# Kernel tuning notes

Measured on AMD Instinct MI355X. Metric: run time of the kernel, lower is better.

## Reference

```python
import jax, jax.numpy as jnp
import numpy as np

# Dimensions (match init_kwargs / input_specs)
B, S, D = 4, 2048, 1024
H, DK = 16, 64
CL = 64            # chunk_len
C, N, NL = 32, 2, 128  # chunks, neighbors, neighbor_len
EPS = 1e-5
SCALE = 1.0 / np.sqrt(DK)


def setup_inputs() -> dict:
    key = jax.random.key(0)
    ks = jax.random.split(key, 8)
    w_in = 1.0 / np.sqrt(D)   # xavier-like scale for projections
    return {
        "h": jax.random.normal(ks[0], (B, S, D), jnp.float32),
        "e": jax.random.normal(ks[1], (B, C, N, NL, D), jnp.float32),
        "ln_g": jnp.ones((D,), jnp.float32),
        "ln_b": jnp.zeros((D,), jnp.float32),
        "Wq": jax.random.normal(ks[2], (D, H * DK), jnp.float32) * w_in,
        "bq": jnp.zeros((H * DK,), jnp.float32),
        "Wk": jax.random.normal(ks[3], (D, H * DK), jnp.float32) * w_in,
        "bk": jnp.zeros((H * DK,), jnp.float32),
        "Wv": jax.random.normal(ks[4], (D, H * DK), jnp.float32) * w_in,
        "bv": jnp.zeros((H * DK,), jnp.float32),
        "Wo": jax.random.normal(ks[5], (H * DK, D), jnp.float32) * (1.0 / np.sqrt(H * DK)),
        "bo": jnp.zeros((D,), jnp.float32),
    }


def _layernorm(x, g, b):
    mu = jnp.mean(x, axis=-1, keepdims=True)
    var = jnp.mean(jnp.square(x - mu), axis=-1, keepdims=True)
    return (x - mu) * jax.lax.rsqrt(var + EPS) * g + b


def reference(h, e, ln_g, ln_b, Wq, bq, Wk, bk, Wv, bv, Wo, bo):
    residual = h
    # shift queries so each chunk attends to neighbors retrieved for the previous chunk
    hs = _layernorm(h[:, CL - 1:], ln_g, ln_b)          # [B, S-CL+1, D]
    total = C * CL
    pad = max(0, total - hs.shape[1])
    hp = jnp.pad(hs, ((0, 0), (0, pad), (0, 0))) if pad > 0 else hs[:, :total]
    hb = hp.reshape(B, C, CL, D)                         # [B,C,CL,D]

    q = (hb @ Wq + bq).reshape(B, C, CL, H, DK)
    k = (e @ Wk + bk).reshape(B, C, N, NL, H, DK)
    v = (e @ Wv + bv).reshape(B, C, N, NL, H, DK)

    # scores: [B, C, H, CL, N, NL], softmax over merged (N, NL)
    attn = jnp.einsum('bcihd,bcnjhd->bchinj', q, k) * SCALE
    sh = attn.shape
    attn = jax.nn.softmax(attn.reshape(sh[0], sh[1], sh[2], sh[3], -1), axis=-1).reshape(sh)

    o = jnp.einsum('bchinj,bcnjhd->bcihd', attn, v).reshape(B, C * CL, H * DK)
    o = o @ Wo + bo                                      # [B, C*CL, D]
    # shift output back and crop to original length
    o = jnp.pad(o, ((0, 0), (CL - 1, 0), (0, 0)))[:, :S]
    return o + residual
```

## Files before the change

kernel.cpp:

```cpp
#include <hip/hip_runtime.h>


typedef __attribute__((ext_vector_type(8))) short short8;
typedef __attribute__((ext_vector_type(4))) float f32x4;
typedef unsigned short ushort_t;
typedef unsigned long long u64;

__device__ inline ushort_t f2bf(float f) {
  union { float f; unsigned int u; } v; v.f = f;
  unsigned int u = v.u;
  return (ushort_t)((u + 0x7fffu + ((u >> 16) & 1u)) >> 16);
}
__device__ inline float bf2f(ushort_t s) {
  union { unsigned int u; float f; } v; v.u = ((unsigned int)s) << 16;
  return v.f;
}

__device__ inline void gl_lds16(const void* g, void* l) {
  __builtin_amdgcn_global_load_lds(
      (const __attribute__((address_space(1))) unsigned int*)g,
      (__attribute__((address_space(3))) unsigned int*)l, 16, 0, 0);
}

__global__ void prep_kernel(const float* __restrict__ W0, const float* __restrict__ W1,
                            const float* __restrict__ W2, const float* __restrict__ W3,
                            ushort_t* __restrict__ T0, ushort_t* __restrict__ T1,
                            ushort_t* __restrict__ T2, ushort_t* __restrict__ T3,
                            const float* __restrict__ h, const float* __restrict__ lg,
                            const float* __restrict__ lb, ushort_t* __restrict__ hb,
                            const float* __restrict__ e, ushort_t* __restrict__ e_bf) {
  __shared__ float tile[32][33];
  __shared__ float red[8];
  const int blk = blockIdx.x, t = threadIdx.x;

  if (blk < 4096) {
    const int z = blk >> 10, xy = blk & 1023;
    const float* W = (z == 0) ? W0 : (z == 1) ? W1 : (z == 2) ? W2 : W3;
    ushort_t* WT   = (z == 0) ? T0 : (z == 1) ? T1 : (z == 2) ? T2 : T3;
    int k0 = (xy & 31) * 32, n0 = (xy >> 5) * 32;
    int c = t & 31, r = t >> 5;
#pragma unroll
    for (int p = 0; p < 4; p++)
      tile[r + p * 8][c] = W[(size_t)(k0 + r + p * 8) * 1024 + n0 + c];
    __syncthreads();
#pragma unroll
    for (int p = 0; p < 4; p++)
      WT[(size_t)(n0 + r + p * 8) * 1024 + k0 + c] = f2bf(tile[c][r + p * 8]);
    return;
  }
  if (blk < 12288) {
    int row = blk - 4096;
    int b = row >> 11, jj = row & 2047;
    ushort_t* dst = hb + (size_t)row * 1024;
    if (jj >= 1985) {
      ((unsigned int*)dst)[t] = 0u;
      ((unsigned int*)dst)[t + 256] = 0u;
      return;
    }
    const float* src = h + ((size_t)(b << 11) + jj + 63) * 1024;
    f32x4 x = *(const f32x4*)&src[t * 4];
    float s = x[0] + x[1] + x[2] + x[3];
    float sq = x[0]*x[0] + x[1]*x[1] + x[2]*x[2] + x[3]*x[3];
#pragma unroll
    for (int off = 32; off > 0; off >>= 1) {
      s  += __shfl_xor(s, off);
      sq += __shfl_xor(sq, off);
    }
    if ((t & 63) == 0) { red[(t >> 6) * 2] = s; red[(t >> 6) * 2 + 1] = sq; }
    __syncthreads();
    float sum = red[0] + red[2] + red[4] + red[6];
    float sumsq = red[1] + red[3] + red[5] + red[7];
    float mu = sum * (1.f / 1024.f);
    float var = sumsq * (1.f / 1024.f) - mu * mu;
    float rs = rsqrtf(var + 1e-5f);
    f32x4 gg = *(const f32x4*)&lg[t * 4];
    f32x4 bv = *(const f32x4*)&lb[t * 4];
    ushort_t o0 = f2bf((x[0] - mu) * rs * gg[0] + bv[0]);
    ushort_t o1 = f2bf((x[1] - mu) * rs * gg[1] + bv[1]);
    ushort_t o2 = f2bf((x[2] - mu) * rs * gg[2] + bv[2]);
    ushort_t o3 = f2bf((x[3] - mu) * rs * gg[3] + bv[3]);
    u64 pack = (u64)o0 | ((u64)o1 << 16) | ((u64)o2 << 32) | ((u64)o3 << 48);
    *(u64*)&dst[t * 4] = pack;
    return;
  }
  {
    int i = (blk - 12288) * 256 + t;
    const f32x4* sp = (const f32x4*)(e + (size_t)i * 8);
    f32x4 a = sp[0], b = sp[1];
    short8 o;
    o[0] = (short)f2bf(a[0]); o[1] = (short)f2bf(a[1]);
    o[2] = (short)f2bf(a[2]); o[3] = (short)f2bf(a[3]);
    o[4] = (short)f2bf(b[0]); o[5] = (short)f2bf(b[1]);
    o[6] = (short)f2bf(b[2]); o[7] = (short)f2bf(b[3]);
    *(short8*)(e_bf + (size_t)i * 8) = o;
  }
}

template <int EPI>
__launch_bounds__(256, 2)
__global__ void gemm_bt(const ushort_t* __restrict__ A, const ushort_t* __restrict__ BT,
                        const float* __restrict__ bias, ushort_t* __restrict__ Cb,
                        float* __restrict__ Cf, const float* __restrict__ resid) {
  const int bid = blockIdx.x;
  if (EPI == 1 && bid >= 512) {
    int tt = bid - 512;
    int b = tt / 63, r = tt % 63;
    size_t idx = ((size_t)(b * 2048) + r) * 1024 + threadIdx.x * 4;
    *(f32x4*)&Cf[idx] = *(const f32x4*)&resid[idx];
    return;
  }
  __shared__ __attribute__((aligned(16))) ushort_t lds[32768];
  const int cpx = 64;
  const int swz = (bid & 7) * cpx + (bid >> 3);
  const int tm = (swz >> 3) * 128, tn = (swz & 7) * 128;
  const int t = threadIdx.x, lane = t & 63, wv = t >> 6;
  const int wm = (wv >> 1) * 64, wn = (wv & 1) * 64;
  const int row16 = lane & 15, g = lane >> 4;

  const int c0 = t, c1 = t + 256;
  const int ra0 = c0 >> 2, sa0 = ((c0 & 3) ^ ((ra0 >> 1) & 3)) * 8;
  const int ra1 = c1 >> 2, sa1 = ((c1 & 3) ^ ((ra1 >> 1) & 3)) * 8;
  const ushort_t* Ag0 = A + (size_t)(tm + ra0) * 1024 + sa0;
  const ushort_t* Ag1 = A + (size_t)(tm + ra1) * 1024 + sa1;
  const ushort_t* Bg0 = BT + (size_t)(tn + ra0) * 1024 + sa0;
  const ushort_t* Bg1 = BT + (size_t)(tn + ra1) * 1024 + sa1;

#define STG_A(T) { ushort_t* L_ = lds + ((T) & 3) * 8192; const int k0_ = (T) * 32; \
    gl_lds16(Ag0 + k0_, L_ + c0 * 8); gl_lds16(Ag1 + k0_, L_ + c1 * 8); }
#define STG_B(T) { ushort_t* L_ = lds + ((T) & 3) * 8192; const int k0_ = (T) * 32; \
    gl_lds16(Bg0 + k0_, L_ + 4096 + c0 * 8); gl_lds16(Bg1 + k0_, L_ + 4096 + c1 * 8); }

  int aoff[4], boff[4];
#pragma unroll
  for (int m = 0; m < 4; m++) {
    int ra = wm + m * 16 + row16;
    aoff[m] = ra * 32 + (g ^ ((ra >> 1) & 3)) * 8;
  }
#pragma unroll
  for (int n = 0; n < 4; n++) {
    int rb = wn + n * 16 + row16;
    boff[n] = 4096 + rb * 32 + (g ^ ((rb >> 1) & 3)) * 8;
  }

  f32x4 acc[4][4] = {};
  STG_A(0); STG_B(0); STG_A(1); STG_B(1);
  for (int T = 0; T < 32; ++T) {
    const ushort_t* Lb = lds + (T & 3) * 8192;
    if (T < 31) { asm volatile("s_waitcnt vmcnt(4)" ::: "memory"); }
    else        { asm volatile("s_waitcnt vmcnt(0)" ::: "memory"); }
    __builtin_amdgcn_s_barrier();
    short8 af0, af1;
    short8 bfv[4];
#pragma unroll
    for (int n = 0; n < 4; n++) bfv[n] = *(const short8*)&Lb[boff[n]];
    af0 = *(const short8*)&Lb[aoff[0]];
    af1 = *(const short8*)&Lb[aoff[1]];
    if (T < 30) STG_A(T + 2);
    __builtin_amdgcn_s_barrier();
    asm volatile("s_waitcnt lgkmcnt(0)" ::: "memory");
    __builtin_amdgcn_sched_barrier(0);
    __builtin_amdgcn_s_setprio(1);
#pragma unroll
    for (int n = 0; n < 4; n++) {
      acc[0][n] = __builtin_amdgcn_mfma_f32_16x16x32_bf16(af0, bfv[n], acc[0][n], 0, 0, 0);
      acc[1][n] = __builtin_amdgcn_mfma_f32_16x16x32_bf16(af1, bfv[n], acc[1][n], 0, 0, 0);
    }
    __builtin_amdgcn_s_setprio(0);
    __builtin_amdgcn_s_barrier();
    af0 = *(const short8*)&Lb[aoff[2]];
    af1 = *(const short8*)&Lb[aoff[3]];
    if (T < 30) STG_B(T + 2);
    __builtin_amdgcn_s_barrier();
    asm volatile("s_waitcnt lgkmcnt(0)" ::: "memory");
    __builtin_amdgcn_sched_barrier(0);
    __builtin_amdgcn_s_setprio(1);
#pragma unroll
    for (int n = 0; n < 4; n++) {
      acc[2][n] = __builtin_amdgcn_mfma_f32_16x16x32_bf16(af0, bfv[n], acc[2][n], 0, 0, 0);
      acc[3][n] = __builtin_amdgcn_mfma_f32_16x16x32_bf16(af1, bfv[n], acc[3][n], 0, 0, 0);
    }
    __builtin_amdgcn_s_setprio(0);
  }
#undef STG_A
#undef STG_B

  const int cr = g * 4, cc = row16;
  if (EPI == 0) {
    const int cb = tn + wn;
    float bsv[4];
#pragma unroll
    for (int n = 0; n < 4; n++) bsv[n] = bias[cb + n * 16 + cc];
#pragma unroll
    for (int m = 0; m < 4; m++) {
      int rbase = tm + wm + m * 16 + cr;
#pragma unroll
      for (int j = 0; j < 4; j++) {
        u64 pack = (u64)f2bf(acc[m][0][j] + bsv[0])
                 | ((u64)f2bf(acc[m][1][j] + bsv[1]) << 16)
                 | ((u64)f2bf(acc[m][2][j] + bsv[2]) << 32)
                 | ((u64)f2bf(acc[m][3][j] + bsv[3]) << 48);
        *(u64*)&Cb[(size_t)(rbase + j) * 1024 + cb + cc * 4] = pack;
      }
    }
  } else {
#pragma unroll
    for (int m = 0; m < 4; m++) {
#pragma unroll
      for (int n = 0; n < 4; n++) {
        int col = tn + wn + n * 16 + cc;
        float bsv = bias[col];
#pragma unroll
        for (int j = 0; j < 4; j++) {
          int rg = tm + wm + m * 16 + cr + j;
          float v = acc[m][n][j] + bsv;
          int b = rg >> 11, jj = rg & 2047;
          if (jj < 1985) {
            size_t oi = ((size_t)(b << 11) + jj + 63) * 1024 + col;
            Cf[oi] = v + resid[oi];
          }
        }
      }
    }
  }
}

__launch_bounds__(512, 2)
__global__ void kv_attn(const ushort_t* __restrict__ A, const ushort_t* __restrict__ WkvT,
                        const float* __restrict__ bk, const float* __restrict__ bv,
                        const ushort_t* __restrict__ Qb, ushort_t* __restrict__ Ob) {
  __shared__ __attribute__((aligned(16))) ushort_t smem[75776];
  ushort_t* lds = smem;
  const int bid = blockIdx.x;
  const int swz = (bid & 7) * 128 + (bid >> 3);
  const int bc = swz >> 3, hp = swz & 7;
  const int tm = bc * 256;
  const int t = threadIdx.x, lane = t & 63, wv = t >> 6;
  const int wm = wv >> 2, wn = wv & 3;
  const int row16 = lane & 15, g = lane >> 4;

  {
    const int hb2q = t >> 8, tlq = t & 255;
    ushort_t* QsH = smem + 67584 + hb2q * 4096;
    size_t qbase = ((size_t)bc * 64) * 1024 + (hp * 2 + hb2q) * 64;
    int ch = tlq, r = ch >> 3, gq = (ch & 7) ^ (r & 7);
    gl_lds16(Qb + qbase + (size_t)r * 1024 + gq * 8, &QsH[ch * 8]);
    ch = tlq + 256; r = ch >> 3; gq = (ch & 7) ^ (r & 7);
    gl_lds16(Qb + qbase + (size_t)r * 1024 + gq * 8, &QsH[ch * 8]);
  }

  const int d1 = t + 512;
  const int ra0 = t >> 2, sa0 = ((t & 3) ^ ((ra0 >> 1) & 3)) * 8;
  const int ra1 = d1 >> 2, sa1 = ((d1 & 3) ^ ((ra1 >> 1) & 3)) * 8;
  const ushort_t* Ag0 = A + (size_t)(tm + ra0) * 1024 + sa0;
  const ushort_t* Ag1 = A + (size_t)(tm + ra1) * 1024 + sa1;
  const ushort_t* Bg0 = WkvT + (size_t)(hp * 128 + ra0) * 1024 + sa0;
  const ushort_t* Bg1 = WkvT + (size_t)(1024 + hp * 128 + (ra1 - 128)) * 1024 + sa1;

#define STG256_A(T) { ushort_t* L_ = lds + ((T) & 3) * 16384; const int k0_ = (T) * 32; \
    gl_lds16(Ag0 + k0_, L_ + t * 8); gl_lds16(Ag1 + k0_, L_ + d1 * 8); }
#define STG256_B(T) { ushort_t* L_ = lds + ((T) & 3) * 16384; const int k0_ = (T) * 32; \
    gl_lds16(Bg0 + k0_, L_ + 8192 + t * 8); gl_lds16(Bg1 + k0_, L_ + 8192 + d1 * 8); }

  int aoff[8], boff[4];
#pragma unroll
  for (int m = 0; m < 8; m++) {
    int ra = wm * 128 + m * 16 + row16;
    aoff[m] = ra * 32 + (g ^ ((ra >> 1) & 3)) * 8;
  }
#pragma unroll
  for (int n = 0; n < 4; n++) {
    int rb = wn * 64 + n * 16 + row16;
    boff[n] = 8192 + rb * 32 + (g ^ ((rb >> 1) & 3)) * 8;
  }

  f32x4 acc[8][4] = {};
  STG256_A(0); STG256_B(0); STG256_A(1); STG256_B(1);
  for (int T = 0; T < 32; ++T) {
    const ushort_t* Lb = lds + (T & 3) * 16384;
    if (T < 31) { asm volatile("s_waitcnt vmcnt(4)" ::: "memory"); }
    else        { asm volatile("s_waitcnt vmcnt(0)" ::: "memory"); }
    __builtin_amdgcn_s_barrier();
    short8 af[4], bfv[4];
#pragma unroll
    for (int n = 0; n < 4; n++) bfv[n] = *(const short8*)&Lb[boff[n]];
#pragma unroll
    for (int m = 0; m < 4; m++) af[m] = *(const short8*)&Lb[aoff[m]];
    if (T < 30) STG256_A(T + 2);
    __builtin_amdgcn_s_barrier();
    asm volatile("s_waitcnt lgkmcnt(0)" ::: "memory");
    __builtin_amdgcn_sched_barrier(0);
    __builtin_amdgcn_s_setprio(1);
#pragma unroll
    for (int m = 0; m < 4; m++)
#pragma unroll
      for (int n = 0; n < 4; n++)
        acc[m][n] = __builtin_amdgcn_mfma_f32_16x16x32_bf16(af[m], bfv[n], acc[m][n], 0, 0, 0);
    __builtin_amdgcn_s_setprio(0);
    __builtin_amdgcn_s_barrier();
#pragma unroll
    for (int m = 0; m < 4; m++) af[m] = *(const short8*)&Lb[aoff[4 + m]];
    if (T < 30) STG256_B(T + 2);
    __builtin_amdgcn_s_barrier();
    asm volatile("s_waitcnt lgkmcnt(0)" ::: "memory");
    __builtin_amdgcn_sched_barrier(0);
    __builtin_amdgcn_s_setprio(1);
#pragma unroll
    for (int m = 0; m < 4; m++)
#pragma unroll
      for (int n = 0; n < 4; n++)
        acc[4 + m][n] = __builtin_amdgcn_mfma_f32_16x16x32_bf16(af[m], bfv[n], acc[4 + m][n], 0, 0, 0);
    __builtin_amdgcn_s_setprio(0);
  }
#undef STG256_A
#undef STG256_B

  __syncthreads();

  if (wn < 2) {
    ushort_t* KsH = smem + wn * 16896;
    float bsv[4];
#pragma unroll
    for (int n = 0; n < 4; n++) bsv[n] = bk[hp * 128 + wn * 64 + n * 16 + row16];
#pragma unroll
    for (int m = 0; m < 8; m++) {
      int krow0 = wm * 128 + m * 16 + g * 4;
#pragma unroll
      for (int j = 0; j < 4; j++) {
        int krow = krow0 + j;
        u64 pack = (u64)f2bf(acc[m][0][j] + bsv[0])
                 | ((u64)f2bf(acc[m][1][j] + bsv[1]) << 16)
                 | ((u64)f2bf(acc[m][2][j] + bsv[2]) << 32)
                 | ((u64)f2bf(acc[m][3][j] + bsv[3]) << 48);
        int sl = ((row16 >> 1) ^ (krow & 7)) * 8 + (row16 & 1) * 4;
        *(u64*)&KsH[krow * 64 + sl] = pack;
      }
    }
  } else {
    ushort_t* VtH = smem + 33792 + (wn & 1) * 16896;
    float bsv[4];
#pragma unroll
    for (int n = 0; n < 4; n++) bsv[n] = bv[hp * 128 + (wn - 2) * 64 + n * 16 + row16];
#pragma unroll
    for (int m = 0; m < 8; m++) {
      int krow0 = wm * 128 + m * 16 + g * 4;
#pragma unroll
      for (int n = 0; n < 4; n++) {
        int od = n * 16 + row16;
        u64 pack = (u64)f2bf(acc[m][n][0] + bsv[n])
                 | ((u64)f2bf(acc[m][n][1] + bsv[n]) << 16)
                 | ((u64)f2bf(acc[m][n][2] + bsv[n]) << 32)
                 | ((u64)f2bf(acc[m][n][3] + bsv[n]) << 48);
        *(u64*)&VtH[od * 264 + krow0] = pack;
      }
    }
  }
  __syncthreads();

  const int tl = t & 255, hb2 = t >> 8;
  const int wvL = tl >> 6, laneL = tl & 63;
  ushort_t* QsH = smem + 67584 + hb2 * 4096;
  ushort_t* KsH = smem + hb2 * 16896;
  ushort_t* SpH = KsH;
  ushort_t* VtH = smem + 33792 + hb2 * 16896;

  const int rowA = laneL & 15, kgA = (laneL >> 4) * 8;
  const int cswz = (rowA & 7) << 3;
  f32x4 accs[4][4] = {};
#pragma unroll
  for (int kk = 0; kk < 64; kk += 32) {
    int cq = ((kk + kgA) ^ cswz);
    short8 af[4], bfr[4];
#pragma unroll
    for (int m = 0; m < 4; m++) af[m] = *(const short8*)&QsH[(m * 16 + rowA) * 64 + cq];
#pragma unroll
    for (int n = 0; n < 4; n++)
      bfr[n] = *(const short8*)&KsH[(wvL * 64 + n * 16 + rowA) * 64 + cq];
#pragma unroll
    for (int m = 0; m < 4; m++)
#pragma unroll
      for (int n = 0; n < 4; n++)
        accs[m][n] = __builtin_amdgcn_mfma_f32_16x16x32_bf16(af[m], bfr[n], accs[m][n], 0, 0, 0);
  }
  __syncthreads();

  {
    const int cr = (laneL >> 4) * 4, cc = laneL & 15;
#pragma unroll
    for (int m = 0; m < 4; m++)
#pragma unroll
      for (int n = 0; n < 4; n++)
#pragma unroll
        for (int j = 0; j < 4; j++)
          SpH[(m * 16 + cr + j) * 264 + wvL * 64 + n * 16 + cc] = f2bf(accs[m][n][j]);
  }
  __syncthreads();

  {
    const int r = tl >> 2, q = tl & 3;
    const int base = r * 264 + q * 64;
    float ev[64];
#pragma unroll
    for (int p = 0; p < 8; p++) {
      short8 sv = *(const short8*)&SpH[base + p * 8];
#pragma unroll
      for (int i = 0; i < 8; i++) ev[p * 8 + i] = bf2f((ushort_t)sv[i]);
    }
    float mx = ev[0];
#pragma unroll
    for (int i = 1; i < 64; i++) mx = fmaxf(mx, ev[i]);
    mx = fmaxf(mx, __shfl_xor(mx, 1));
    mx = fmaxf(mx, __shfl_xor(mx, 2));
    float sum = 0.f;
#pragma unroll
    for (int i = 0; i < 64; i++) {
      ev[i] = __expf((ev[i] - mx) * 0.125f);
      sum += ev[i];
    }
    sum += __shfl_xor(sum, 1);
    sum += __shfl_xor(sum, 2);
    float inv = 1.f / sum;
#pragma unroll
    for (int p = 0; p < 8; p++) {
      short8 pv;
#pragma unroll
      for (int i = 0; i < 8; i++) pv[i] = (short)f2bf(ev[p * 8 + i] * inv);
      *(short8*)&SpH[base + p * 8] = pv;
    }
  }
  __syncthreads();

  {
    f32x4 acco[4] = {};
#pragma unroll
    for (int kt = 0; kt < 8; kt++) {
      short8 bfv = *(const short8*)&VtH[(wvL * 16 + rowA) * 264 + kt * 32 + kgA];
#pragma unroll
      for (int m = 0; m < 4; m++) {
        short8 af = *(const short8*)&SpH[(m * 16 + rowA) * 264 + kt * 32 + kgA];
        acco[m] = __builtin_amdgcn_mfma_f32_16x16x32_bf16(af, bfv, acco[m], 0, 0, 0);
      }
    }
    const int cr = (laneL >> 4) * 4, cc = laneL & 15;
    size_t obase = ((size_t)bc * 64) * 1024 + (hp * 2 + hb2) * 64 + wvL * 16 + cc;
#pragma unroll
    for (int m = 0; m < 4; m++)
#pragma unroll
      for (int j = 0; j < 4; j++)
        Ob[obase + (size_t)(m * 16 + cr + j) * 1024] = f2bf(acco[m][j]);
  }
}

extern "C" void kernel_launch(void* const* d_in, const int* in_sizes, int n_in,
                              void* d_out, int out_size, void* d_ws, size_t ws_size,
                              hipStream_t stream) {
  const float* h    = (const float*)d_in[0];
  const float* e    = (const float*)d_in[1];
  const float* ln_g = (const float*)d_in[2];
  const float* ln_b = (const float*)d_in[3];
  const float* Wq   = (const float*)d_in[4];
  const float* bq   = (const float*)d_in[5];
  const float* Wk   = (const float*)d_in[6];
  const float* bk   = (const float*)d_in[7];
  const float* Wv   = (const float*)d_in[8];
  const float* bv   = (const float*)d_in[9];
  const float* Wo   = (const float*)d_in[10];
  const float* bo   = (const float*)d_in[11];
  float* out = (float*)d_out;

  char* ws = (char*)d_ws;
  const size_t MB = 1024 * 1024;
  ushort_t* WqT  = (ushort_t*)(ws + 0 * MB);
  ushort_t* WkT  = (ushort_t*)(ws + 2 * MB);
  ushort_t* WvT  = (ushort_t*)(ws + 4 * MB);
  ushort_t* WoT  = (ushort_t*)(ws + 6 * MB);
  ushort_t* hb   = (ushort_t*)(ws + 8 * MB);
  ushort_t* e_bf = (ushort_t*)(ws + 24 * MB);
  ushort_t* Qb   = (ushort_t*)(ws + 88 * MB);
  ushort_t* Obuf = (ushort_t*)(ws + 104 * MB);

  prep_kernel<<<28672, 256, 0, stream>>>(Wq, Wk, Wv, Wo, WqT, WkT, WvT, WoT,
                                         h, ln_g, ln_b, hb, e, e_bf);

  gemm_bt<0><<<512, 256, 0, stream>>>(hb, WqT, bq, Qb, nullptr, nullptr);
  kv_attn<<<1024, 512, 0, stream>>>(e_bf, WkT, bk, bv, Qb, Obuf);

  gemm_bt<1><<<764, 256, 0, stream>>>(Obuf, WoT, bo, nullptr, out, h);
}
```

Measured before the change: 258.4 us.

## Load K/V weight fragments straight to registers instead of staging through LDS

In the fused K/V projection GEMM loop, the weight (B) operand is now fetched with direct global-to-register loads into a pair of register buffers, prefetched one k-tile ahead. Only the activation (A) tile is still staged through LDS, which halves the per-stage LDS footprint and removes the B-side LDS writes and reads. The loop is unrolled by two so the even and odd register buffers alternate, and the vmcnt waits are retuned for the new load counts. In exchange, waves that share the same column block now issue duplicate global loads of strided weight rows, and B-load latency must be hidden by a single tile of prefetch.

```diff
diff --git a/kernel.cpp b/kernel.cpp
--- a/kernel.cpp
+++ b/kernel.cpp
@@ -253,66 +253,74 @@
   const int ra1 = d1 >> 2, sa1 = ((d1 & 3) ^ ((ra1 >> 1) & 3)) * 8;
   const ushort_t* Ag0 = A + (size_t)(tm + ra0) * 1024 + sa0;
   const ushort_t* Ag1 = A + (size_t)(tm + ra1) * 1024 + sa1;
-  const ushort_t* Bg0 = WkvT + (size_t)(hp * 128 + ra0) * 1024 + sa0;
-  const ushort_t* Bg1 = WkvT + (size_t)(1024 + hp * 128 + (ra1 - 128)) * 1024 + sa1;
-
-#define STG256_A(T) { ushort_t* L_ = lds + ((T) & 3) * 16384; const int k0_ = (T) * 32; \
+
+#define STG256_A(T) { ushort_t* L_ = lds + ((T) & 3) * 8192; const int k0_ = (T) * 32; \
     gl_lds16(Ag0 + k0_, L_ + t * 8); gl_lds16(Ag1 + k0_, L_ + d1 * 8); }
-#define STG256_B(T) { ushort_t* L_ = lds + ((T) & 3) * 16384; const int k0_ = (T) * 32; \
-    gl_lds16(Bg0 + k0_, L_ + 8192 + t * 8); gl_lds16(Bg1 + k0_, L_ + 8192 + d1 * 8); }
-
-  int aoff[8], boff[4];
+
+  int aoff[8];
 #pragma unroll
   for (int m = 0; m < 8; m++) {
     int ra = wm * 128 + m * 16 + row16;
     aoff[m] = ra * 32 + (g ^ ((ra >> 1) & 3)) * 8;
   }
+
+  const ushort_t* Bbase[4];
 #pragma unroll
   for (int n = 0; n < 4; n++) {
     int rb = wn * 64 + n * 16 + row16;
-    boff[n] = 8192 + rb * 32 + (g ^ ((rb >> 1) & 3)) * 8;
-  }
-
+    int grow = (rb < 128) ? (hp * 128 + rb) : (1024 + hp * 128 + (rb - 128));
+    Bbase[n] = WkvT + (size_t)grow * 1024 + g * 8;
+  }
+#define LDB(T, R) { const int k0_ = (T) * 32;                                  \
+    _Pragma("unroll")                                                          \
+    for (int n_ = 0; n_ < 4; n_++) R[n_] = *(const short8*)(Bbase[n_] + k0_); }
+
+  short8 bfvE[4], bfvO[4];
   f32x4 acc[8][4] = {};
-  STG256_A(0); STG256_B(0); STG256_A(1); STG256_B(1);
-  for (int T = 0; T < 32; ++T) {
-    const ushort_t* Lb = lds + (T & 3) * 16384;
-    if (T < 31) { asm volatile("s_waitcnt vmcnt(4)" ::: "memory"); }
-    else        { asm volatile("s_waitcnt vmcnt(0)" ::: "memory"); }
-    __builtin_amdgcn_s_barrier();
-    short8 af[4], bfv[4];
-#pragma unroll
-    for (int n = 0; n < 4; n++) bfv[n] = *(const short8*)&Lb[boff[n]];
-#pragma unroll
-    for (int m = 0; m < 4; m++) af[m] = *(const short8*)&Lb[aoff[m]];
-    if (T < 30) STG256_A(T + 2);
-    __builtin_amdgcn_s_barrier();
-    asm volatile("s_waitcnt lgkmcnt(0)" ::: "memory");
-    __builtin_amdgcn_sched_barrier(0);
-    __builtin_amdgcn_s_setprio(1);
-#pragma unroll
-    for (int m = 0; m < 4; m++)
-#pragma unroll
-      for (int n = 0; n < 4; n++)
-        acc[m][n] = __builtin_amdgcn_mfma_f32_16x16x32_bf16(af[m], bfv[n], acc[m][n], 0, 0, 0);
-    __builtin_amdgcn_s_setprio(0);
-    __builtin_amdgcn_s_barrier();
-#pragma unroll
-    for (int m = 0; m < 4; m++) af[m] = *(const short8*)&Lb[aoff[4 + m]];
-    if (T < 30) STG256_B(T + 2);
-    __builtin_amdgcn_s_barrier();
-    asm volatile("s_waitcnt lgkmcnt(0)" ::: "memory");
-    __builtin_amdgcn_sched_barrier(0);
-    __builtin_amdgcn_s_setprio(1);
-#pragma unroll
-    for (int m = 0; m < 4; m++)
-#pragma unroll
-      for (int n = 0; n < 4; n++)
-        acc[4 + m][n] = __builtin_amdgcn_mfma_f32_16x16x32_bf16(af[m], bfv[n], acc[4 + m][n], 0, 0, 0);
-    __builtin_amdgcn_s_setprio(0);
-  }
+  STG256_A(0); LDB(0, bfvE); STG256_A(1);
+
+#define KV_TILE(T, BCUR, BNXT, VMC)                                           \
+  { asm volatile("s_waitcnt vmcnt(" #VMC ")" ::: "memory");                   \
+    __builtin_amdgcn_s_barrier();                                             \
+    const ushort_t* Lb = lds + ((T) & 3) * 8192;                              \
+    short8 af_[4];                                                            \
+    _Pragma("unroll")                                                         \
+    for (int m_ = 0; m_ < 4; m_++) af_[m_] = *(const short8*)&Lb[aoff[m_]];   \
+    if ((T) < 31) { LDB((T) + 1, BNXT); }                                     \
+    if ((T) < 30) { STG256_A((T) + 2); }                                      \
+    __builtin_amdgcn_s_barrier();                                             \
+    asm volatile("s_waitcnt lgkmcnt(0)" ::: "memory");                        \
+    __builtin_amdgcn_sched_barrier(0);                                        \
+    __builtin_amdgcn_s_setprio(1);                                            \
+    _Pragma("unroll")                                                         \
+    for (int m_ = 0; m_ < 4; m_++)                                            \
+      _Pragma("unroll")                                                       \
+      for (int n_ = 0; n_ < 4; n_++)                                          \
+        acc[m_][n_] = __builtin_amdgcn_mfma_f32_16x16x32_bf16(af_[m_], BCUR[n_], acc[m_][n_], 0, 0, 0); \
+    __builtin_amdgcn_s_setprio(0);                                            \
+    __builtin_amdgcn_s_barrier();                                             \
+    _Pragma("unroll")                                                         \
+    for (int m_ = 0; m_ < 4; m_++) af_[m_] = *(const short8*)&Lb[aoff[4 + m_]]; \
+    __builtin_amdgcn_s_barrier();                                             \
+    asm volatile("s_waitcnt lgkmcnt(0)" ::: "memory");                        \
+    __builtin_amdgcn_sched_barrier(0);                                        \
+    __builtin_amdgcn_s_setprio(1);                                            \
+    _Pragma("unroll")                                                         \
+    for (int m_ = 0; m_ < 4; m_++)                                            \
+      _Pragma("unroll")                                                       \
+      for (int n_ = 0; n_ < 4; n_++)                                          \
+        acc[4 + m_][n_] = __builtin_amdgcn_mfma_f32_16x16x32_bf16(af_[m_], BCUR[n_], acc[4 + m_][n_], 0, 0, 0); \
+    __builtin_amdgcn_s_setprio(0); }
+
+  for (int it = 0; it < 15; ++it) {
+    KV_TILE(2 * it,     bfvE, bfvO, 2);
+    KV_TILE(2 * it + 1, bfvO, bfvE, 2);
+  }
+  KV_TILE(30, bfvE, bfvO, 2);
+  KV_TILE(31, bfvO, bfvE, 0);
+#undef KV_TILE
+#undef LDB
 #undef STG256_A
-#undef STG256_B
 
   __syncthreads();
 
```

New measurement: 334.3 us. 1.29x slower.

## Restructure KV projection mainloop to K=64 double-buffered stages

Applied to the files above, without the earlier changes.

Replaces the 4-stage K=32 ring buffer and its split A/B staging and 8-wave ping-pong barriers with a 2-stage double buffer holding 64-wide K tiles. Each iteration waits for all outstanding loads, issues the next stage's global-to-LDS copies, then runs two K=32 sub-steps over all 8x4 MFMA tiles. The LDS swizzle changes to XOR across 8 chunks per row. This halves the barriers per unit of K and lengthens MFMA runs, at the cost of a full vmcnt(0) wait each iteration, which may expose load latency that the deeper pipeline used to hide.

```diff
diff --git a/kernel.cpp b/kernel.cpp
--- a/kernel.cpp
+++ b/kernel.cpp
@@ -248,71 +248,64 @@
     gl_lds16(Qb + qbase + (size_t)r * 1024 + gq * 8, &QsH[ch * 8]);
   }
 
-  const int d1 = t + 512;
-  const int ra0 = t >> 2, sa0 = ((t & 3) ^ ((ra0 >> 1) & 3)) * 8;
-  const int ra1 = d1 >> 2, sa1 = ((d1 & 3) ^ ((ra1 >> 1) & 3)) * 8;
-  const ushort_t* Ag0 = A + (size_t)(tm + ra0) * 1024 + sa0;
-  const ushort_t* Ag1 = A + (size_t)(tm + ra1) * 1024 + sa1;
-  const ushort_t* Bg0 = WkvT + (size_t)(hp * 128 + ra0) * 1024 + sa0;
-  const ushort_t* Bg1 = WkvT + (size_t)(1024 + hp * 128 + (ra1 - 128)) * 1024 + sa1;
-
-#define STG256_A(T) { ushort_t* L_ = lds + ((T) & 3) * 16384; const int k0_ = (T) * 32; \
-    gl_lds16(Ag0 + k0_, L_ + t * 8); gl_lds16(Ag1 + k0_, L_ + d1 * 8); }
-#define STG256_B(T) { ushort_t* L_ = lds + ((T) & 3) * 16384; const int k0_ = (T) * 32; \
-    gl_lds16(Bg0 + k0_, L_ + 8192 + t * 8); gl_lds16(Bg1 + k0_, L_ + 8192 + d1 * 8); }
-
-  int aoff[8], boff[4];
-#pragma unroll
-  for (int m = 0; m < 8; m++) {
-    int ra = wm * 128 + m * 16 + row16;
-    aoff[m] = ra * 32 + (g ^ ((ra >> 1) & 3)) * 8;
-  }
-#pragma unroll
-  for (int n = 0; n < 4; n++) {
-    int rb = wn * 64 + n * 16 + row16;
-    boff[n] = 8192 + rb * 32 + (g ^ ((rb >> 1) & 3)) * 8;
+  const ushort_t* Agp[4];
+  const ushort_t* Bgp[4];
+  int destC[4];
+#pragma unroll
+  for (int p = 0; p < 4; p++) {
+    int c = t + 512 * p;
+    int r = c >> 3, s = c & 7;
+    int srck = (s ^ (r & 7)) * 8;
+    destC[p] = c * 8;
+    Agp[p] = A + (size_t)(tm + r) * 1024 + srck;
+    int grow = (r < 128) ? (hp * 128 + r) : (1024 + hp * 128 + (r - 128));
+    Bgp[p] = WkvT + (size_t)grow * 1024 + srck;
+  }
+#define STG64(T) { ushort_t* L_ = lds + ((T) & 1) * 32768; const int k0_ = (T) * 64; \
+    gl_lds16(Agp[0] + k0_, L_ + destC[0]); gl_lds16(Agp[1] + k0_, L_ + destC[1]); \
+    gl_lds16(Agp[2] + k0_, L_ + destC[2]); gl_lds16(Agp[3] + k0_, L_ + destC[3]); \
+    gl_lds16(Bgp[0] + k0_, L_ + 16384 + destC[0]); gl_lds16(Bgp[1] + k0_, L_ + 16384 + destC[1]); \
+    gl_lds16(Bgp[2] + k0_, L_ + 16384 + destC[2]); gl_lds16(Bgp[3] + k0_, L_ + 16384 + destC[3]); }
+
+  int aoffk[2][8], boffk[2][4];
+#pragma unroll
+  for (int kk2 = 0; kk2 < 2; kk2++) {
+#pragma unroll
+    for (int m = 0; m < 8; m++) {
+      int ra = wm * 128 + m * 16 + row16;
+      aoffk[kk2][m] = ra * 64 + (((g + 4 * kk2)) ^ (ra & 7)) * 8;
+    }
+#pragma unroll
+    for (int n = 0; n < 4; n++) {
+      int rb = wn * 64 + n * 16 + row16;
+      boffk[kk2][n] = 16384 + rb * 64 + (((g + 4 * kk2)) ^ (rb & 7)) * 8;
+    }
   }
 
   f32x4 acc[8][4] = {};
-  STG256_A(0); STG256_B(0); STG256_A(1); STG256_B(1);
-  for (int T = 0; T < 32; ++T) {
-    const ushort_t* Lb = lds + (T & 3) * 16384;
-    if (T < 31) { asm volatile("s_waitcnt vmcnt(4)" ::: "memory"); }
-    else        { asm volatile("s_waitcnt vmcnt(0)" ::: "memory"); }
+  STG64(0);
+  for (int T = 0; T < 16; ++T) {
+    asm volatile("s_waitcnt vmcnt(0)" ::: "memory");
     __builtin_amdgcn_s_barrier();
-    short8 af[4], bfv[4];
-#pragma unroll
-    for (int n = 0; n < 4; n++) bfv[n] = *(const short8*)&Lb[boff[n]];
-#pragma unroll
-    for (int m = 0; m < 4; m++) af[m] = *(const short8*)&Lb[aoff[m]];
-    if (T < 30) STG256_A(T + 2);
-    __builtin_amdgcn_s_barrier();
-    asm volatile("s_waitcnt lgkmcnt(0)" ::: "memory");
-    __builtin_amdgcn_sched_barrier(0);
-    __builtin_amdgcn_s_setprio(1);
-#pragma unroll
-    for (int m = 0; m < 4; m++)
-#pragma unroll
-      for (int n = 0; n < 4; n++)
-        acc[m][n] = __builtin_amdgcn_mfma_f32_16x16x32_bf16(af[m], bfv[n], acc[m][n], 0, 0, 0);
-    __builtin_amdgcn_s_setprio(0);
-    __builtin_amdgcn_s_barrier();
-#pragma unroll
-    for (int m = 0; m < 4; m++) af[m] = *(const short8*)&Lb[aoff[4 + m]];
-    if (T < 30) STG256_B(T + 2);
-    __builtin_amdgcn_s_barrier();
-    asm volatile("s_waitcnt lgkmcnt(0)" ::: "memory");
-    __builtin_amdgcn_sched_barrier(0);
-    __builtin_amdgcn_s_setprio(1);
-#pragma unroll
-    for (int m = 0; m < 4; m++)
-#pragma unroll
-      for (int n = 0; n < 4; n++)
-        acc[4 + m][n] = __builtin_amdgcn_mfma_f32_16x16x32_bf16(af[m], bfv[n], acc[4 + m][n], 0, 0, 0);
-    __builtin_amdgcn_s_setprio(0);
-  }
-#undef STG256_A
-#undef STG256_B
+    if (T < 15) STG64(T + 1);
+    const ushort_t* Lb = lds + (T & 1) * 32768;
+#pragma unroll
+    for (int kk2 = 0; kk2 < 2; kk2++) {
+      short8 af[8], bfv[4];
+#pragma unroll
+      for (int n = 0; n < 4; n++) bfv[n] = *(const short8*)&Lb[boffk[kk2][n]];
+#pragma unroll
+      for (int m = 0; m < 8; m++) af[m] = *(const short8*)&Lb[aoffk[kk2][m]];
+      __builtin_amdgcn_s_setprio(1);
+#pragma unroll
+      for (int m = 0; m < 8; m++)
+#pragma unroll
+        for (int n = 0; n < 4; n++)
+          acc[m][n] = __builtin_amdgcn_mfma_f32_16x16x32_bf16(af[m], bfv[n], acc[m][n], 0, 0, 0);
+      __builtin_amdgcn_s_setprio(0);
+    }
+  }
+#undef STG64
 
   __syncthreads();
 
```

Result: faster. 249.3 us (-3.5%).
